# Kernel tuning notes

Hardware: AMD Instinct MI355X
Metric: run time of the kernel (lower is better)

## Reference

```python
import jax, jax.numpy as jnp
import numpy as np

B, T, C, H = 2, 2048, 1024, 16
HD = C // H  # head dim = 64


def setup_inputs() -> dict:
    key = jax.random.key(0)
    k1, k2, k3, k4, k5 = jax.random.split(key, 5)
    s = 0.02
    return {
        "x": jax.random.normal(k1, (B, T, C), dtype=jnp.float32),
        "W_attn": jax.random.normal(k2, (3 * C, C), dtype=jnp.float32) * s,
        "b_attn": jax.random.normal(k3, (3 * C,), dtype=jnp.float32) * s,
        "W_proj": jax.random.normal(k4, (C, C), dtype=jnp.float32) * s,
        "b_proj": jax.random.normal(k5, (C,), dtype=jnp.float32) * s,
    }


def reference(x, W_attn, b_attn, W_proj, b_proj):
    Bs, Ts, Cs = x.shape
    # QKV projection (torch Linear: x @ W.T + b)
    qkv = x @ W_attn.T + b_attn  # (B, T, 3C)
    q, k, v = jnp.split(qkv, 3, axis=2)
    # (B, H, T, HD)
    q = q.reshape(Bs, Ts, H, HD).transpose(0, 2, 1, 3)
    k = k.reshape(Bs, Ts, H, HD).transpose(0, 2, 1, 3)
    v = v.reshape(Bs, Ts, H, HD).transpose(0, 2, 1, 3)
    scale = 1.0 / np.sqrt(HD).astype(np.float32)
    att = jnp.einsum("bhqd,bhkd->bhqk", q, k) * scale
    causal = jnp.tril(jnp.ones((Ts, Ts), dtype=bool))
    att = jnp.where(causal[None, None], att, -jnp.inf)
    att = jax.nn.softmax(att, axis=-1)
    y = jnp.einsum("bhqk,bhkd->bhqd", att, v)
    y = y.transpose(0, 2, 1, 3).reshape(Bs, Ts, Cs)
    return y @ W_proj.T + b_proj
```

## Files before the change

### kernel.cpp

```cpp
#include <hip/hip_runtime.h>


#define B_   2
#define T_   2048
#define C_   1024
#define H_   16
#define HD_  64
#define BT_  (B_ * T_)
#define C3_  (3 * C_)
#define NT_  (T_ / 64)

typedef __attribute__((ext_vector_type(8))) __bf16 bf16x8;
typedef __attribute__((ext_vector_type(4))) float  f32x4;
typedef __attribute__((ext_vector_type(8))) unsigned short u16x8;

__device__ __forceinline__ unsigned short f2bf(float f) {
    unsigned int u = __float_as_uint(f);
    u = (u + 0x7fffu + ((u >> 16) & 1u)) >> 16;
    return (unsigned short)u;
}
__device__ __forceinline__ unsigned short bfc(float f) {
    return __builtin_bit_cast(unsigned short, (__bf16)f);
}

#define GLOAD16(g, l) __builtin_amdgcn_global_load_lds(                          \
    (const __attribute__((address_space(1))) unsigned int*)(g),                  \
    (__attribute__((address_space(3))) unsigned int*)(l), 16, 0, 0)

#define NX8  (BT_ * C_ / 8)
#define NWA8 (C3_ * C_ / 8)
#define NWP8 (C_ * C_ / 8)
__global__ __launch_bounds__(256) void cvt3(const float* __restrict__ x,
                                            const float* __restrict__ wa,
                                            const float* __restrict__ wp,
                                            unsigned short* __restrict__ ox,
                                            unsigned short* __restrict__ owa,
                                            unsigned short* __restrict__ owp) {
    int i = blockIdx.x * 256 + threadIdx.x;
    const float* in;
    unsigned short* out;
    int j;
    if (i < NX8)             { in = x;  out = ox;  j = i; }
    else if (i < NX8 + NWA8) { in = wa; out = owa; j = i - NX8; }
    else                     { in = wp; out = owp; j = i - NX8 - NWA8; }
    const float4* p = (const float4*)in;
    float4 f0 = p[j * 2];
    float4 f1 = p[j * 2 + 1];
    u16x8 o;
    o[0] = f2bf(f0.x); o[1] = f2bf(f0.y); o[2] = f2bf(f0.z); o[3] = f2bf(f0.w);
    o[4] = f2bf(f1.x); o[5] = f2bf(f1.y); o[6] = f2bf(f1.z); o[7] = f2bf(f1.w);
    ((u16x8*)out)[j] = o;
}

template<int OUT_BF16>
__global__ __launch_bounds__(256) void gemm_lds(const unsigned short* __restrict__ A,
                                                const unsigned short* __restrict__ Bm,
                                                const float* __restrict__ bias,
                                                void* __restrict__ Cv,
                                                int M, int N, int K) {
    __shared__ __align__(16) unsigned short As[128][64];
    __shared__ __align__(16) unsigned short Bs[128][64];

    const int t    = threadIdx.x;
    const int lane = t & 63;
    const int w    = t >> 6;
    const int wr   = w & 1;
    const int wc   = w >> 1;
    const int l15  = lane & 15;
    const int lhi  = lane >> 4;
    const int m0   = blockIdx.y * 128;
    const int n0   = blockIdx.x * 128;
    const int lr8  = lane >> 3;
    const int lc8  = (lane & 7) * 8;

    f32x4 acc[4][4] = {};

    for (int kb = 0; kb < K; kb += 64) {
        __syncthreads();
        #pragma unroll
        for (int i = 0; i < 4; ++i) {
            const int row = w * 32 + i * 8;
            GLOAD16(A  + (size_t)(m0 + row + lr8) * K + kb + lc8, &As[row][0]);
            GLOAD16(Bm + (size_t)(n0 + row + lr8) * K + kb + lc8, &Bs[row][0]);
        }
        __syncthreads();
        #pragma unroll
        for (int kk = 0; kk < 2; ++kk) {
            bf16x8 af[4], bfm[4];
            #pragma unroll
            for (int m = 0; m < 4; ++m)
                af[m] = *(const bf16x8*)(&As[wr * 64 + m * 16 + l15][kk * 32 + lhi * 8]);
            #pragma unroll
            for (int n = 0; n < 4; ++n)
                bfm[n] = *(const bf16x8*)(&Bs[wc * 64 + n * 16 + l15][kk * 32 + lhi * 8]);
            #pragma unroll
            for (int m = 0; m < 4; ++m)
                #pragma unroll
                for (int n = 0; n < 4; ++n)
                    acc[m][n] = __builtin_amdgcn_mfma_f32_16x16x32_bf16(af[m], bfm[n], acc[m][n], 0, 0, 0);
        }
    }

    #pragma unroll
    for (int n = 0; n < 4; ++n) {
        int cg = n0 + wc * 64 + n * 16 + l15;
        float bv = bias[cg];
        #pragma unroll
        for (int m = 0; m < 4; ++m) {
            #pragma unroll
            for (int i = 0; i < 4; ++i) {
                int rg  = m0 + wr * 64 + m * 16 + lhi * 4 + i;
                float v = acc[m][n][i] + bv;
                if (OUT_BF16)
                    ((unsigned short*)Cv)[(size_t)rg * N + cg] = f2bf(v);
                else
                    ((float*)Cv)[(size_t)rg * N + cg] = v;
            }
        }
    }
}

__global__ __launch_bounds__(256) void attn_fwd(const unsigned short* __restrict__ qkv,
                                                unsigned short* __restrict__ y) {
    __shared__ __align__(16) unsigned short Ks[128][72];
    __shared__ __align__(16) unsigned short Vt[64][136];

    const int t    = threadIdx.x;
    const int lane = t & 63;
    const int wv   = t >> 6;
    const int l15  = lane & 15;
    const int lhi  = lane >> 4;
    const int b    = blockIdx.y >> 4;
    const int h    = blockIdx.y & 15;
    const size_t rowbase = (size_t)b * T_ * C3_;
    const int hoff = h * HD_;
    unsigned short* PsW = &Ks[0][0] + wv * (16 * 136);

    const unsigned short* krow  = qkv + rowbase + C_ + hoff;
    const unsigned short* vbase = qkv + rowbase + 2 * C_ + hoff;
    const int vm = t >> 2;
    const int vc = t & 3;
    const float SCL = 0.18033688f;

    #pragma unroll 1
    for (int half = 0; half < 2; ++half) {
        const int qt = half ? (NT_ - 1 - (int)blockIdx.x) : (int)blockIdx.x;
        const int q0 = qt * 64;

        bf16x8 qf[2];
        {
            int qrow = q0 + wv * 16 + l15;
            const unsigned short* qp = qkv + rowbase + (size_t)qrow * C3_ + hoff + lhi * 8;
            qf[0] = *(const bf16x8*)(qp);
            qf[1] = *(const bf16x8*)(qp + 32);
        }

        float Mx = -1e30f, Lx = 0.f;
        f32x4 oacc[4];
        #pragma unroll
        for (int n = 0; n < 4; ++n) oacc[n] = f32x4{0.f, 0.f, 0.f, 0.f};

        const int niter = (qt + 2) >> 1;
        for (int it = 0; it < niter; ++it) {
            const int k0 = it * 128;
            __syncthreads();
            #pragma unroll
            for (int i = 0; i < 4; ++i) {
                int g   = i * 256 + t;
                int row = g >> 3;
                int kc  = g & 7;
                *(uint4*)(&Ks[row][kc * 8]) =
                    *(const uint4*)(krow + (size_t)(k0 + row) * C3_ + kc * 8);
            }
            {
                const unsigned short* r0 = vbase + (size_t)(k0 + 2 * vm) * C3_ + vc * 16;
                const unsigned short* r1 = r0 + C3_;
                u16x8 a0 = *(const u16x8*)(r0);
                u16x8 a1 = *(const u16x8*)(r0 + 8);
                u16x8 b0 = *(const u16x8*)(r1);
                u16x8 b1 = *(const u16x8*)(r1 + 8);
                #pragma unroll
                for (int i = 0; i < 8; ++i) {
                    *(unsigned int*)(&Vt[vc * 16 + i][2 * vm]) =
                        (unsigned int)a0[i] | ((unsigned int)b0[i] << 16);
                    *(unsigned int*)(&Vt[vc * 16 + 8 + i][2 * vm]) =
                        (unsigned int)a1[i] | ((unsigned int)b1[i] << 16);
                }
            }
            __syncthreads();

            f32x4 sacc[8];
            #pragma unroll
            for (int n = 0; n < 8; ++n) sacc[n] = f32x4{0.f, 0.f, 0.f, 0.f};
            __builtin_amdgcn_s_setprio(1);
            #pragma unroll
            for (int kk = 0; kk < 2; ++kk) {
                #pragma unroll
                for (int n = 0; n < 8; ++n) {
                    bf16x8 kf = *(const bf16x8*)(&Ks[n * 16 + l15][kk * 32 + lhi * 8]);
                    sacc[n] = __builtin_amdgcn_mfma_f32_16x16x32_bf16(kf, qf[kk], sacc[n], 0, 0, 0);
                }
            }
            __builtin_amdgcn_s_setprio(0);
            __syncthreads();

            const int qg = q0 + wv * 16 + l15;
            if (k0 + 127 <= q0) {
                #pragma unroll
                for (int n = 0; n < 8; ++n)
                    #pragma unroll
                    for (int r = 0; r < 4; ++r)
                        sacc[n][r] *= SCL;
            } else {
                #pragma unroll
                for (int n = 0; n < 8; ++n) {
                    int kg = k0 + n * 16 + lhi * 4;
                    #pragma unroll
                    for (int r = 0; r < 4; ++r)
                        sacc[n][r] = (kg + r <= qg) ? sacc[n][r] * SCL : -1e30f;
                }
            }

            float vmx = sacc[0][0];
            #pragma unroll
            for (int n = 0; n < 8; ++n)
                #pragma unroll
                for (int r = 0; r < 4; ++r) vmx = fmaxf(vmx, sacc[n][r]);
            vmx = fmaxf(vmx, __shfl_xor(vmx, 16));
            vmx = fmaxf(vmx, __shfl_xor(vmx, 32));
            float Mn = fmaxf(Mx, vmx);
            float al = exp2f(Mx - Mn);
            Mx = Mn;
            float rs = 0.f;
            #pragma unroll
            for (int n = 0; n < 8; ++n)
                #pragma unroll
                for (int r = 0; r < 4; ++r) {
                    float e = exp2f(sacc[n][r] - Mn);
                    sacc[n][r] = e;
                    rs += e;
                }
            rs += __shfl_xor(rs, 16);
            rs += __shfl_xor(rs, 32);
            Lx = Lx * al + rs;

            #pragma unroll
            for (int r = 0; r < 4; ++r) {
                float ar = __shfl(al, lhi * 4 + r);
                #pragma unroll
                for (int nd = 0; nd < 4; ++nd) oacc[nd][r] *= ar;
            }

            #pragma unroll
            for (int n = 0; n < 8; ++n) {
                unsigned int lo = (unsigned int)bfc(sacc[n][0]) | ((unsigned int)bfc(sacc[n][1]) << 16);
                unsigned int hi = (unsigned int)bfc(sacc[n][2]) | ((unsigned int)bfc(sacc[n][3]) << 16);
                uint2 pk; pk.x = lo; pk.y = hi;
                *(uint2*)(PsW + l15 * 136 + n * 16 + lhi * 4) = pk;
            }
            asm volatile("s_waitcnt lgkmcnt(0)" ::: "memory");

            __builtin_amdgcn_s_setprio(1);
            #pragma unroll
            for (int kk = 0; kk < 4; ++kk) {
                bf16x8 pf = *(const bf16x8*)(PsW + l15 * 136 + kk * 32 + lhi * 8);
                #pragma unroll
                for (int nd = 0; nd < 4; ++nd) {
                    bf16x8 vf = *(const bf16x8*)(&Vt[nd * 16 + l15][kk * 32 + lhi * 8]);
                    oacc[nd] = __builtin_amdgcn_mfma_f32_16x16x32_bf16(pf, vf, oacc[nd], 0, 0, 0);
                }
            }
            __builtin_amdgcn_s_setprio(0);
        }

        #pragma unroll
        for (int i = 0; i < 4; ++i) {
            float Lr = __shfl(Lx, lhi * 4 + i);
            float rL = 1.0f / Lr;
            #pragma unroll
            for (int nd = 0; nd < 4; ++nd) {
                int qg = q0 + wv * 16 + lhi * 4 + i;
                y[(size_t)(b * T_ + qg) * C_ + hoff + nd * 16 + l15] = bfc(oacc[nd][i] * rL);
            }
        }
    }
}

extern "C" void kernel_launch(void* const* d_in, const int* in_sizes, int n_in,
                              void* d_out, int out_size, void* d_ws, size_t ws_size,
                              hipStream_t stream) {
    const float* x      = (const float*)d_in[0];
    const float* W_attn = (const float*)d_in[1];
    const float* b_attn = (const float*)d_in[2];
    const float* W_proj = (const float*)d_in[3];
    const float* b_proj = (const float*)d_in[4];
    float* out = (float*)d_out;

    char* ws = (char*)d_ws;
    unsigned short* xb   = (unsigned short*)(ws);
    unsigned short* wab  = (unsigned short*)(ws + 8388608);
    unsigned short* wpb  = (unsigned short*)(ws + 8388608 + 6291456);
    unsigned short* qkvb = (unsigned short*)(ws + 16777216);
    unsigned short* yb   = (unsigned short*)(ws + 16777216 + 25165824);

    cvt3<<<(NX8 + NWA8 + NWP8) / 256, 256, 0, stream>>>(x, W_attn, W_proj, xb, wab, wpb);

    gemm_lds<1><<<dim3(C3_ / 128, BT_ / 128), 256, 0, stream>>>(xb, wab, b_attn, qkvb, BT_, C3_, C_);

    attn_fwd<<<dim3(NT_ / 2, B_ * H_), 256, 0, stream>>>(qkvb, yb);

    gemm_lds<0><<<dim3(C_ / 128, BT_ / 128), 256, 0, stream>>>(yb, wpb, b_proj, out, BT_, C_, C_);
}
```

Baseline: 220.9 us.

## Store V transposed from QKV GEMM, fold softmax scale into weights, remap GEMM grid

The QKV GEMM epilogue now writes the V columns in a per-head transposed layout inside the V slots of the qkv buffer, so attention loads V^T straight into LDS with vector loads instead of transposing it through scattered 32-bit LDS writes. The softmax scale (with its log2e factor) is folded into the Q weights and bias during the conversion kernel, which removes the per-element multiply in attention. The GEMM drops the direct global-to-LDS loads for register-staged loads into padded LDS tiles, and it remaps block indices in an XCD-aware order. The V epilogue stores are strided 8-byte writes, which may hurt GEMM store efficiency.

```diff
diff --git a/kernel.cpp b/kernel.cpp
--- a/kernel.cpp
+++ b/kernel.cpp
@@ -9,6 +9,7 @@
 #define BT_  (B_ * T_)
 #define C3_  (3 * C_)
 #define NT_  (T_ / 64)
+#define SCL_ 0.18033688f
 
 typedef __attribute__((ext_vector_type(8))) __bf16 bf16x8;
 typedef __attribute__((ext_vector_type(4))) float  f32x4;
@@ -23,43 +24,61 @@
     return __builtin_bit_cast(unsigned short, (__bf16)f);
 }
 
-#define GLOAD16(g, l) __builtin_amdgcn_global_load_lds(                          \
-    (const __attribute__((address_space(1))) unsigned int*)(g),                  \
-    (__attribute__((address_space(3))) unsigned int*)(l), 16, 0, 0)
+__device__ __forceinline__ size_t vphys(size_t idx) {
+    return (idx >> 10) * 3072 + 2048 + (idx & 1023);
+}
 
 #define NX8  (BT_ * C_ / 8)
 #define NWA8 (C3_ * C_ / 8)
 #define NWP8 (C_ * C_ / 8)
+#define NB8  (C3_ / 8)
+#define NTOT (NX8 + NWA8 + NWP8 + NB8)
 __global__ __launch_bounds__(256) void cvt3(const float* __restrict__ x,
                                             const float* __restrict__ wa,
                                             const float* __restrict__ wp,
+                                            const float* __restrict__ ba,
                                             unsigned short* __restrict__ ox,
                                             unsigned short* __restrict__ owa,
-                                            unsigned short* __restrict__ owp) {
+                                            unsigned short* __restrict__ owp,
+                                            float* __restrict__ obs) {
     int i = blockIdx.x * 256 + threadIdx.x;
+    if (i >= NTOT) return;
+    if (i >= NX8 + NWA8 + NWP8) {
+        int jb = i - (NX8 + NWA8 + NWP8);
+        int e  = jb * 8;
+        float s = (e < C_) ? SCL_ : 1.0f;
+        const float4* p = (const float4*)(ba + e);
+        float4 f0 = p[0], f1 = p[1];
+        float4* o = (float4*)(obs + e);
+        o[0] = make_float4(f0.x * s, f0.y * s, f0.z * s, f0.w * s);
+        o[1] = make_float4(f1.x * s, f1.y * s, f1.z * s, f1.w * s);
+        return;
+    }
     const float* in;
     unsigned short* out;
     int j;
+    float s = 1.0f;
     if (i < NX8)             { in = x;  out = ox;  j = i; }
-    else if (i < NX8 + NWA8) { in = wa; out = owa; j = i - NX8; }
+    else if (i < NX8 + NWA8) { in = wa; out = owa; j = i - NX8;
+                               if (j < NWP8) s = SCL_; }
     else                     { in = wp; out = owp; j = i - NX8 - NWA8; }
     const float4* p = (const float4*)in;
     float4 f0 = p[j * 2];
     float4 f1 = p[j * 2 + 1];
     u16x8 o;
-    o[0] = f2bf(f0.x); o[1] = f2bf(f0.y); o[2] = f2bf(f0.z); o[3] = f2bf(f0.w);
-    o[4] = f2bf(f1.x); o[5] = f2bf(f1.y); o[6] = f2bf(f1.z); o[7] = f2bf(f1.w);
+    o[0] = f2bf(f0.x * s); o[1] = f2bf(f0.y * s); o[2] = f2bf(f0.z * s); o[3] = f2bf(f0.w * s);
+    o[4] = f2bf(f1.x * s); o[5] = f2bf(f1.y * s); o[6] = f2bf(f1.z * s); o[7] = f2bf(f1.w * s);
     ((u16x8*)out)[j] = o;
 }
 
-template<int OUT_BF16>
-__global__ __launch_bounds__(256) void gemm_lds(const unsigned short* __restrict__ A,
-                                                const unsigned short* __restrict__ Bm,
-                                                const float* __restrict__ bias,
-                                                void* __restrict__ Cv,
-                                                int M, int N, int K) {
-    __shared__ __align__(16) unsigned short As[128][64];
-    __shared__ __align__(16) unsigned short Bs[128][64];
+template<int OUT_BF16, int VSPLIT>
+__global__ __launch_bounds__(256) void gemm_bt(const unsigned short* __restrict__ A,
+                                               const unsigned short* __restrict__ Bm,
+                                               const float* __restrict__ bias,
+                                               void* __restrict__ Cv,
+                                               int M, int N, int K, int nbx) {
+    __shared__ __align__(16) unsigned short As[128][72];
+    __shared__ __align__(16) unsigned short Bs[128][72];
 
     const int t    = threadIdx.x;
     const int lane = t & 63;
@@ -68,20 +87,29 @@
     const int wc   = w >> 1;
     const int l15  = lane & 15;
     const int lhi  = lane >> 4;
-    const int m0   = blockIdx.y * 128;
-    const int n0   = blockIdx.x * 128;
-    const int lr8  = lane >> 3;
-    const int lc8  = (lane & 7) * 8;
+
+    const int nwg = gridDim.x;
+    const int q8  = nwg >> 3;
+    const int lin = (int)(blockIdx.x & 7) * q8 + (int)(blockIdx.x >> 3);
+    const int bx  = lin % nbx;
+    const int by  = lin / nbx;
+    const int m0  = by * 128;
+    const int n0  = bx * 128;
 
     f32x4 acc[4][4] = {};
 
-    for (int kb = 0; kb < K; kb += 64) {
+    const int nk = K >> 6;
+    for (int kb = 0; kb < nk; ++kb) {
         __syncthreads();
         #pragma unroll
         for (int i = 0; i < 4; ++i) {
-            const int row = w * 32 + i * 8;
-            GLOAD16(A  + (size_t)(m0 + row + lr8) * K + kb + lc8, &As[row][0]);
-            GLOAD16(Bm + (size_t)(n0 + row + lr8) * K + kb + lc8, &Bs[row][0]);
+            int g   = i * 256 + t;
+            int row = g >> 3;
+            int kc  = g & 7;
+            uint4 va = *(const uint4*)(A  + (size_t)(m0 + row) * K + kb * 64 + kc * 8);
+            *(uint4*)(&As[row][kc * 8]) = va;
+            uint4 vb = *(const uint4*)(Bm + (size_t)(n0 + row) * K + kb * 64 + kc * 8);
+            *(uint4*)(&Bs[row][kc * 8]) = vb;
         }
         __syncthreads();
         #pragma unroll
@@ -101,20 +129,45 @@
         }
     }
 
-    #pragma unroll
-    for (int n = 0; n < 4; ++n) {
-        int cg = n0 + wc * 64 + n * 16 + l15;
-        float bv = bias[cg];
-        #pragma unroll
-        for (int m = 0; m < 4; ++m) {
-            #pragma unroll
-            for (int i = 0; i < 4; ++i) {
-                int rg  = m0 + wr * 64 + m * 16 + lhi * 4 + i;
-                float v = acc[m][n][i] + bv;
-                if (OUT_BF16)
-                    ((unsigned short*)Cv)[(size_t)rg * N + cg] = f2bf(v);
-                else
-                    ((float*)Cv)[(size_t)rg * N + cg] = v;
+    if (VSPLIT && n0 >= 2048) {
+        #pragma unroll
+        for (int n = 0; n < 4; ++n) {
+            int cg = n0 + wc * 64 + n * 16 + l15;
+            float bv = bias[cg];
+            int d_ = cg - 2048;
+            int hh = d_ >> 6;
+            int dd = d_ & 63;
+            #pragma unroll
+            for (int m = 0; m < 4; ++m) {
+                int rg0 = m0 + wr * 64 + m * 16 + lhi * 4;
+                int bb  = rg0 >> 11;
+                int tt  = rg0 & 2047;
+                size_t idx = ((size_t)((bb * 16 + hh) * 64 + dd)) * 2048 + tt;
+                unsigned short* dst = (unsigned short*)Cv + vphys(idx);
+                uint2 pk;
+                pk.x = (unsigned int)f2bf(acc[m][n][0] + bv) |
+                       ((unsigned int)f2bf(acc[m][n][1] + bv) << 16);
+                pk.y = (unsigned int)f2bf(acc[m][n][2] + bv) |
+                       ((unsigned int)f2bf(acc[m][n][3] + bv) << 16);
+                *(uint2*)dst = pk;
+            }
+        }
+    } else {
+        #pragma unroll
+        for (int n = 0; n < 4; ++n) {
+            int cg = n0 + wc * 64 + n * 16 + l15;
+            float bv = bias[cg];
+            #pragma unroll
+            for (int m = 0; m < 4; ++m) {
+                #pragma unroll
+                for (int i = 0; i < 4; ++i) {
+                    int rg  = m0 + wr * 64 + m * 16 + lhi * 4 + i;
+                    float v = acc[m][n][i] + bv;
+                    if (OUT_BF16)
+                        ((unsigned short*)Cv)[(size_t)rg * N + cg] = f2bf(v);
+                    else
+                        ((float*)Cv)[(size_t)rg * N + cg] = v;
+                }
             }
         }
     }
@@ -136,11 +189,8 @@
     const int hoff = h * HD_;
     unsigned short* PsW = &Ks[0][0] + wv * (16 * 136);
 
-    const unsigned short* krow  = qkv + rowbase + C_ + hoff;
-    const unsigned short* vbase = qkv + rowbase + 2 * C_ + hoff;
-    const int vm = t >> 2;
-    const int vc = t & 3;
-    const float SCL = 0.18033688f;
+    const unsigned short* krow = qkv + rowbase + C_ + hoff;
+    const size_t vIdx0 = ((size_t)(b * 16 + h) * 64) * 2048;
 
     #pragma unroll 1
     for (int half = 0; half < 2; ++half) {
@@ -172,20 +222,13 @@
                 *(uint4*)(&Ks[row][kc * 8]) =
                     *(const uint4*)(krow + (size_t)(k0 + row) * C3_ + kc * 8);
             }
-            {
-                const unsigned short* r0 = vbase + (size_t)(k0 + 2 * vm) * C3_ + vc * 16;
-                const unsigned short* r1 = r0 + C3_;
-                u16x8 a0 = *(const u16x8*)(r0);
-                u16x8 a1 = *(const u16x8*)(r0 + 8);
-                u16x8 b0 = *(const u16x8*)(r1);
-                u16x8 b1 = *(const u16x8*)(r1 + 8);
-                #pragma unroll
-                for (int i = 0; i < 8; ++i) {
-                    *(unsigned int*)(&Vt[vc * 16 + i][2 * vm]) =
-                        (unsigned int)a0[i] | ((unsigned int)b0[i] << 16);
-                    *(unsigned int*)(&Vt[vc * 16 + 8 + i][2 * vm]) =
-                        (unsigned int)a1[i] | ((unsigned int)b1[i] << 16);
-                }
+            #pragma unroll
+            for (int i = 0; i < 4; ++i) {
+                int g  = i * 256 + t;
+                int dd = g >> 4;
+                int kc = g & 15;
+                size_t idx = vIdx0 + (size_t)dd * 2048 + k0 + kc * 8;
+                *(u16x8*)(&Vt[dd][kc * 8]) = *(const u16x8*)(qkv + vphys(idx));
             }
             __syncthreads();
 
@@ -205,19 +248,13 @@
             __syncthreads();
 
             const int qg = q0 + wv * 16 + l15;
-            if (k0 + 127 <= q0) {
-                #pragma unroll
-                for (int n = 0; n < 8; ++n)
-                    #pragma unroll
-                    for (int r = 0; r < 4; ++r)
-                        sacc[n][r] *= SCL;
-            } else {
+            if (k0 + 127 > q0) {
                 #pragma unroll
                 for (int n = 0; n < 8; ++n) {
                     int kg = k0 + n * 16 + lhi * 4;
                     #pragma unroll
                     for (int r = 0; r < 4; ++r)
-                        sacc[n][r] = (kg + r <= qg) ? sacc[n][r] * SCL : -1e30f;
+                        sacc[n][r] = (kg + r <= qg) ? sacc[n][r] : -1e30f;
                 }
             }
 
@@ -302,12 +339,13 @@
     unsigned short* wpb  = (unsigned short*)(ws + 8388608 + 6291456);
     unsigned short* qkvb = (unsigned short*)(ws + 16777216);
     unsigned short* yb   = (unsigned short*)(ws + 16777216 + 25165824);
-
-    cvt3<<<(NX8 + NWA8 + NWP8) / 256, 256, 0, stream>>>(x, W_attn, W_proj, xb, wab, wpb);
-
-    gemm_lds<1><<<dim3(C3_ / 128, BT_ / 128), 256, 0, stream>>>(xb, wab, b_attn, qkvb, BT_, C3_, C_);
+    float*          bs   = (float*)(ws + 16777216 + 25165824 + 8388608);
+
+    cvt3<<<(NTOT + 255) / 256, 256, 0, stream>>>(x, W_attn, W_proj, b_attn, xb, wab, wpb, bs);
+
+    gemm_bt<1, 1><<<(C3_ / 128) * (BT_ / 128), 256, 0, stream>>>(xb, wab, bs, qkvb, BT_, C3_, C_, C3_ / 128);
 
     attn_fwd<<<dim3(NT_ / 2, B_ * H_), 256, 0, stream>>>(qkvb, yb);
 
-    gemm_lds<0><<<dim3(C_ / 128, BT_ / 128), 256, 0, stream>>>(yb, wpb, b_proj, out, BT_, C_, C_);
-}
+    gemm_bt<0, 0><<<(C_ / 128) * (BT_ / 128), 256, 0, stream>>>(yb, wpb, b_proj, out, BT_, C_, C_, C_ / 128);
+}
```

Measured after the change: 211.0 us. 1.05x faster.
